# Kernel tuning notes

Hardware: AMD Instinct MI355X
Metric: run time of the kernel (lower is better)

The kernel has to match this reference:

```python
import jax, jax.numpy as jnp
import numpy as np

N, E, IN, H, HEADS, L, OUT = 4096, 262144, 64, 128, 4, 2, 2
DH = H // HEADS  # 32, per-head dim for both GAT and global MHA
BN_EPS = 1e-5
NEG_SLOPE = 0.2  # GATConv leaky_relu default


def setup_inputs() -> dict:
    key = jax.random.key(0)
    ks = iter(jax.random.split(key, 32))
    rn = lambda shape, s: jax.random.normal(next(ks), shape, jnp.float32) * s
    return {
        "x": rn((N, IN), 1.0),
        "edge_index": jax.random.randint(next(ks), (2, E), 0, N),
        "w_in": rn((H, IN), IN ** -0.5),
        "b_in": rn((H,), 0.02),
        "w_gat": rn((L, H, H), H ** -0.5),
        "att_src": rn((L, HEADS, DH), 0.1),
        "att_dst": rn((L, HEADS, DH), 0.1),
        "b_gat": rn((L, H), 0.02),
        "w_qkv": rn((L, 3 * H, H), H ** -0.5),
        "b_qkv": rn((L, 3 * H), 0.02),
        "w_o": rn((L, H, H), H ** -0.5),
        "b_o": rn((L, H), 0.02),
        "bn_gamma": 1.0 + rn((L, 3, H), 0.05),
        "bn_beta": rn((L, 3, H), 0.05),
        "w1": rn((L, 2 * H, H), H ** -0.5),
        "b1": rn((L, 2 * H), 0.02),
        "w2": rn((L, H, 2 * H), (2 * H) ** -0.5),
        "b2": rn((L, H), 0.02),
        "w_out": rn((OUT, H), H ** -0.5),
        "b_out": rn((OUT,), 0.02),
    }


def _bn(h, g, b):
    # eval-mode BatchNorm1d with running_mean=0, running_var=1
    return h * (g / jnp.sqrt(1.0 + BN_EPS)) + b


def _gat(x, src, dst, w, a_src, a_dst, bias):
    # GATConv(hidden, hidden//heads, heads=HEADS, add_self_loops=False), concat=True
    xp = (x @ w.T).reshape(N, HEADS, DH)                  # [N, HEADS, DH]
    al_s = jnp.einsum('nhd,hd->nh', xp, a_src)            # [N, HEADS]
    al_d = jnp.einsum('nhd,hd->nh', xp, a_dst)
    logit = al_s[src] + al_d[dst]                         # [E, HEADS]
    logit = jnp.where(logit >= 0, logit, NEG_SLOPE * logit)
    m = jax.ops.segment_max(logit, dst, num_segments=N)   # scatter-softmax over dst
    m = jnp.where(jnp.isfinite(m), m, 0.0)
    e = jnp.exp(logit - m[dst])
    denom = jax.ops.segment_sum(e, dst, num_segments=N)
    alpha = e / (denom[dst] + 1e-16)
    out = jax.ops.segment_sum(alpha[:, :, None] * xp[src], dst, num_segments=N)
    return out.reshape(N, H) + bias


def _mha(x, wqkv, bqkv, wo, bo):
    # torch.nn.MultiheadAttention self-attention over all N nodes (one graph)
    qkv = x @ wqkv.T + bqkv
    q, k, v = jnp.split(qkv, 3, axis=-1)
    q = q.reshape(N, HEADS, DH)
    k = k.reshape(N, HEADS, DH)
    v = v.reshape(N, HEADS, DH)
    scores = jnp.einsum('nhd,mhd->hnm', q, k) / jnp.sqrt(jnp.float32(DH))
    attn = jax.nn.softmax(scores, axis=-1)
    out = jnp.einsum('hnm,mhd->nhd', attn, v).reshape(N, H)
    return out @ wo.T + bo


def reference(x, edge_index, w_in, b_in, w_gat, att_src, att_dst, b_gat,
              w_qkv, b_qkv, w_o, b_o, bn_gamma, bn_beta,
              w1, b1, w2, b2, w_out, b_out):
    src, dst = edge_index[0], edge_index[1]
    h = jax.nn.relu(x @ w_in.T + b_in)
    for l in range(L):
        # GPSConv: local GAT branch (dropout inactive in eval)
        h_loc = _gat(h, src, dst, w_gat[l], att_src[l], att_dst[l], b_gat[l]) + h
        h_loc = _bn(h_loc, bn_gamma[l, 0], bn_beta[l, 0])
        # GPSConv: global attention branch
        h_att = _mha(h, w_qkv[l], b_qkv[l], w_o[l], b_o[l]) + h
        h_att = _bn(h_att, bn_gamma[l, 1], bn_beta[l, 1])
        out = h_loc + h_att
        mlp = jax.nn.relu(out @ w1[l].T + b1[l]) @ w2[l].T + b2[l]
        out = _bn(out + mlp, bn_gamma[l, 2], bn_beta[l, 2])
        # GPSRiskModel residual + relu (dropout inactive in eval)
        h = jax.nn.relu(out + h)
    return h @ w_out.T + b_out
```

## Files before the change

### kernel.cpp

```cpp
#include <hip/hip_runtime.h>

#define NN 4096
#define EE 262144
#define INF_ 64
#define HH 128
#define HEADS 4
#define DH 32
#define LL 2
#define NH (NN * HH)
#define KSPLIT 8
#define L2E 1.4426950408889634f

typedef unsigned short u16;
typedef unsigned int u32;
using bf16x8 = __attribute__((ext_vector_type(8))) short;
using f32x4 = __attribute__((ext_vector_type(4))) float;

__device__ __forceinline__ float bf2f(u16 v) { return __uint_as_float(((u32)v) << 16); }
__device__ __forceinline__ u16 f2bf(float f) {
    u32 u = __float_as_uint(f);
    u32 r = (u + 0x7fffu + ((u >> 16) & 1u)) >> 16;
    return (u16)r;
}
__device__ __forceinline__ u32 encf(float f) {
    u32 b = __float_as_uint(f);
    return (b & 0x80000000u) ? ~b : (b | 0x80000000u);
}
__device__ __forceinline__ float decf(u32 u) {
    u32 b = (u & 0x80000000u) ? (u & 0x7fffffffu) : ~u;
    return __uint_as_float(b);
}

__global__ __launch_bounds__(256) void k_detect(const u16* __restrict__ x, int* __restrict__ flag,
                                                int* __restrict__ cnt, u32* __restrict__ gmax) {
    int t = threadIdx.x;
    for (int i = t; i < NN; i += 256) cnt[i] = 0;
    if (t < 16) gmax[t] = 0;
    __shared__ int cs[256];
    u16 v = x[2 * t];
    int e = (v >> 7) & 0xFF;
    cs[t] = (e >= 100 && e <= 140) ? 1 : 0;
    __syncthreads();
    for (int s = 128; s > 0; s >>= 1) {
        if (t < s) cs[t] += cs[t + s];
        __syncthreads();
    }
    if (t == 0) *flag = (cs[0] >= 128) ? 1 : 0;
}

#define MAXSEG 16
struct SegF { const void* src[MAXSEG]; int dst[MAXSEG]; int n[MAXSEG]; int cnt; };
__global__ void k_cvtf(SegF S, float* __restrict__ W, const int* __restrict__ flag) {
    int seg = blockIdx.y;
    if (seg >= S.cnt) return;
    int n = S.n[seg];
    float* d = W + S.dst[seg];
    const void* s = S.src[seg];
    int f = *flag;
    for (int i = blockIdx.x * 256 + threadIdx.x; i < n; i += gridDim.x * 256)
        d[i] = f ? bf2f(((const u16*)s)[i]) : ((const float*)s)[i];
}
struct SegB { const void* src[8]; u16* dst[8]; u16* dst2[8]; int n[8]; int cnt; };
__global__ void k_cvtb(SegB S, const int* __restrict__ flag) {
    int seg = blockIdx.y;
    if (seg >= S.cnt) return;
    int n = S.n[seg];
    u16* d = S.dst[seg];
    u16* d2 = S.dst2[seg];
    const void* s = S.src[seg];
    int f = *flag;
    for (int i = blockIdx.x * 256 + threadIdx.x; i < n; i += gridDim.x * 256) {
        if (d2) {
            float v = f ? bf2f(((const u16*)s)[i]) : ((const float*)s)[i];
            u16 h = f2bf(v);
            d[i] = h;
            d2[i] = f2bf(v - bf2f(h));
        } else {
            d[i] = f ? ((const u16*)s)[i] : f2bf(((const float*)s)[i]);
        }
    }
}

__global__ void k_hist(const int* __restrict__ dst, int* __restrict__ cnt) {
    int e = blockIdx.x * blockDim.x + threadIdx.x;
    if (e < EE) atomicAdd(&cnt[dst[e]], 1);
}
__global__ __launch_bounds__(256) void k_scan(const int* __restrict__ cnt, int* __restrict__ rowstart,
                                              int* __restrict__ cursor) {
    __shared__ int part[256];
    int t = threadIdx.x;
    int loc[16];
    int s = 0;
#pragma unroll
    for (int i = 0; i < 16; ++i) { loc[i] = s; s += cnt[t * 16 + i]; }
    part[t] = s;
    __syncthreads();
    for (int off = 1; off < 256; off <<= 1) {
        int v = part[t];
        int a = (t >= off) ? part[t - off] : 0;
        __syncthreads();
        part[t] = v + a;
        __syncthreads();
    }
    int base = (t == 0) ? 0 : part[t - 1];
#pragma unroll
    for (int i = 0; i < 16; ++i) {
        rowstart[t * 16 + i] = base + loc[i];
        cursor[t * 16 + i] = base + loc[i];
    }
}
__global__ void k_scatter(const int* __restrict__ src, const int* __restrict__ dst,
                          int* __restrict__ cursor, int* __restrict__ esrc) {
    int e = blockIdx.x * blockDim.x + threadIdx.x;
    if (e < EE) {
        int d = dst[e];
        int p = atomicAdd(&cursor[d], 1);
        esrc[p] = src[e];
    }
}

__global__ __launch_bounds__(128) void k_mgemm(const u16* __restrict__ Ahi, const u16* __restrict__ Alo,
                                               const u16* __restrict__ Wb, const float* __restrict__ bias,
                                               float* __restrict__ outf, u16* __restrict__ outb16,
                                               u16* __restrict__ outhi, u16* __restrict__ outlo,
                                               int K, int J, int relu) {
    int wave = threadIdx.x >> 6, lane = threadIdx.x & 63;
    int grp = lane >> 4, lcol = lane & 15;
    int m0 = blockIdx.x * 32 + wave * 16;
    int j0 = blockIdx.y * 64;
    f32x4 acc[4];
#pragma unroll
    for (int s = 0; s < 4; ++s) acc[s] = (f32x4){0.f, 0.f, 0.f, 0.f};
    const u16* ah = Ahi + (size_t)(m0 + lcol) * K + grp * 8;
    const u16* al = Alo + (size_t)(m0 + lcol) * K + grp * 8;
    const u16* wb = Wb + (size_t)(j0 + lcol) * K + grp * 8;
    for (int k = 0; k < K; k += 32) {
        bf16x8 va = *(const bf16x8*)(ah + k);
        bf16x8 vl = *(const bf16x8*)(al + k);
#pragma unroll
        for (int s = 0; s < 4; ++s) {
            bf16x8 vw = *(const bf16x8*)(wb + (size_t)s * 16 * K + k);
            acc[s] = __builtin_amdgcn_mfma_f32_16x16x32_bf16(va, vw, acc[s], 0, 0, 0);
            acc[s] = __builtin_amdgcn_mfma_f32_16x16x32_bf16(vl, vw, acc[s], 0, 0, 0);
        }
    }
#pragma unroll
    for (int s = 0; s < 4; ++s) {
        int col = j0 + s * 16 + lcol;
        float bs = bias ? bias[col] : 0.f;
#pragma unroll
        for (int r = 0; r < 4; ++r) {
            float v = acc[s][r] + bs;
            if (relu) v = fmaxf(v, 0.f);
            size_t idx = (size_t)(m0 + grp * 4 + r) * J + col;
            if (outf) outf[idx] = v;
            if (outb16) outb16[idx] = f2bf(v);
            if (outhi) {
                u16 hv = f2bf(v);
                outhi[idx] = hv;
                outlo[idx] = f2bf(v - bf2f(hv));
            }
        }
    }
}

__global__ __launch_bounds__(128) void k_gemm_gq(const u16* __restrict__ Ahi, const u16* __restrict__ Alo,
                                                 const u16* __restrict__ wgat, const u16* __restrict__ wqkv,
                                                 const float* __restrict__ bqkv,
                                                 float* __restrict__ xpf, u16* __restrict__ xpb,
                                                 u16* __restrict__ qkvb) {
    int wave = threadIdx.x >> 6, lane = threadIdx.x & 63;
    int grp = lane >> 4, lcol = lane & 15;
    int m0 = blockIdx.x * 32 + wave * 16;
    int jb = blockIdx.y;
    int j0 = jb * 64;
    const u16* Wb = (jb < 2) ? (wgat + (size_t)j0 * HH) : (wqkv + (size_t)(j0 - 128) * HH);
    f32x4 acc[4];
#pragma unroll
    for (int s = 0; s < 4; ++s) acc[s] = (f32x4){0.f, 0.f, 0.f, 0.f};
    const u16* ah = Ahi + (size_t)(m0 + lcol) * HH + grp * 8;
    const u16* al = Alo + (size_t)(m0 + lcol) * HH + grp * 8;
    const u16* wb = Wb + (size_t)lcol * HH + grp * 8;
    for (int k = 0; k < HH; k += 32) {
        bf16x8 va = *(const bf16x8*)(ah + k);
        bf16x8 vl = *(const bf16x8*)(al + k);
#pragma unroll
        for (int s = 0; s < 4; ++s) {
            bf16x8 vw = *(const bf16x8*)(wb + (size_t)s * 16 * HH + k);
            acc[s] = __builtin_amdgcn_mfma_f32_16x16x32_bf16(va, vw, acc[s], 0, 0, 0);
            acc[s] = __builtin_amdgcn_mfma_f32_16x16x32_bf16(vl, vw, acc[s], 0, 0, 0);
        }
    }
    if (jb < 2) {
#pragma unroll
        for (int s = 0; s < 4; ++s) {
            int col = j0 + s * 16 + lcol;
#pragma unroll
            for (int r = 0; r < 4; ++r) {
                float v = acc[s][r];
                size_t idx = (size_t)(m0 + grp * 4 + r) * HH + col;
                xpf[idx] = v;
                xpb[idx] = f2bf(v);
            }
        }
    } else {
#pragma unroll
        for (int s = 0; s < 4; ++s) {
            int colq = j0 - 128 + s * 16 + lcol;
            float bs = bqkv[colq];
#pragma unroll
            for (int r = 0; r < 4; ++r)
                qkvb[(size_t)(m0 + grp * 4 + r) * 384 + colq] = f2bf(acc[s][r] + bs);
        }
    }
}

__global__ __launch_bounds__(256) void k_attlog(const float* __restrict__ xp, const float* __restrict__ asrc,
                                                const float* __restrict__ adst, float* __restrict__ als,
                                                float* __restrict__ ald, u32* __restrict__ gmax) {
    int t = blockIdx.x * 256 + threadIdx.x;
    int n = t >> 2, hh = t & 3;
    const float* xr = xp + (size_t)n * HH + hh * DH;
    float s1 = 0.f, s2 = 0.f;
#pragma unroll
    for (int d = 0; d < DH; ++d) {
        float v = xr[d];
        s1 += v * asrc[hh * DH + d];
        s2 += v * adst[hh * DH + d];
    }
    als[t] = s1;
    ald[t] = s2;
    __shared__ float red[256];
    int lt = threadIdx.x;
    red[lt] = s1;
    __syncthreads();
    for (int off = 128; off >= 4; off >>= 1) {
        if (lt < off) red[lt] = fmaxf(red[lt], red[lt + off]);
        __syncthreads();
    }
    if (lt < 4) atomicMax(&gmax[lt], encf(red[lt]));
    __syncthreads();
    red[lt] = s2;
    __syncthreads();
    for (int off = 128; off >= 4; off >>= 1) {
        if (lt < off) red[lt] = fmaxf(red[lt], red[lt + off]);
        __syncthreads();
    }
    if (lt < 4) atomicMax(&gmax[4 + lt], encf(red[lt]));
}

__global__ __launch_bounds__(128) void k_gemm_wo(const u16* __restrict__ Ahi, const u16* __restrict__ Alo,
                                                 const u16* __restrict__ Wb, const float* __restrict__ bias,
                                                 const float* __restrict__ gatb, const float* __restrict__ hbuf,
                                                 const float* __restrict__ bgat, const float* __restrict__ gam,
                                                 const float* __restrict__ bet,
                                                 float* __restrict__ outb, u16* __restrict__ ohi,
                                                 u16* __restrict__ olo) {
    int wave = threadIdx.x >> 6, lane = threadIdx.x & 63;
    int grp = lane >> 4, lcol = lane & 15;
    int m0 = blockIdx.x * 32 + wave * 16;
    int j0 = blockIdx.y * 64;
    f32x4 acc[4];
#pragma unroll
    for (int s = 0; s < 4; ++s) acc[s] = (f32x4){0.f, 0.f, 0.f, 0.f};
    const u16* ah = Ahi + (size_t)(m0 + lcol) * HH + grp * 8;
    const u16* al = Alo + (size_t)(m0 + lcol) * HH + grp * 8;
    const u16* wb = Wb + (size_t)(j0 + lcol) * HH + grp * 8;
    for (int k = 0; k < HH; k += 32) {
        bf16x8 va = *(const bf16x8*)(ah + k);
        bf16x8 vl = *(const bf16x8*)(al + k);
#pragma unroll
        for (int s = 0; s < 4; ++s) {
            bf16x8 vw = *(const bf16x8*)(wb + (size_t)s * 16 * HH + k);
            acc[s] = __builtin_amdgcn_mfma_f32_16x16x32_bf16(va, vw, acc[s], 0, 0, 0);
            acc[s] = __builtin_amdgcn_mfma_f32_16x16x32_bf16(vl, vw, acc[s], 0, 0, 0);
        }
    }
    float rs = rsqrtf(1.00001f);
#pragma unroll
    for (int s = 0; s < 4; ++s) {
        int col = j0 + s * 16 + lcol;
        float bs = bias[col];
        float g0 = gam[col] * rs, b0 = bet[col];
        float g1 = gam[HH + col] * rs, b1 = bet[HH + col];
        float bg = bgat[col];
#pragma unroll
        for (int r = 0; r < 4; ++r) {
            size_t idx = (size_t)(m0 + grp * 4 + r) * HH + col;
            float proj = acc[s][r] + bs;
            float hv = hbuf[idx];
            float hl = g0 * (gatb[idx] + bg + hv) + b0;
            float ha = g1 * (proj + hv) + b1;
            float v = hl + ha;
            outb[idx] = v;
            u16 hb = f2bf(v);
            ohi[idx] = hb;
            olo[idx] = f2bf(v - bf2f(hb));
        }
    }
}

__global__ __launch_bounds__(128) void k_gemm_w2(const u16* __restrict__ Ahi, const u16* __restrict__ Alo,
                                                 const u16* __restrict__ Wb, const float* __restrict__ bias,
                                                 const float* __restrict__ outb, const float* __restrict__ gam2,
                                                 const float* __restrict__ bet2,
                                                 float* __restrict__ hbuf, u16* __restrict__ hhi,
                                                 u16* __restrict__ hlo) {
    int wave = threadIdx.x >> 6, lane = threadIdx.x & 63;
    int grp = lane >> 4, lcol = lane & 15;
    int m0 = blockIdx.x * 32 + wave * 16;
    int j0 = blockIdx.y * 64;
    const int K = 2 * HH;
    f32x4 acc[4];
#pragma unroll
    for (int s = 0; s < 4; ++s) acc[s] = (f32x4){0.f, 0.f, 0.f, 0.f};
    const u16* ah = Ahi + (size_t)(m0 + lcol) * K + grp * 8;
    const u16* al = Alo + (size_t)(m0 + lcol) * K + grp * 8;
    const u16* wb = Wb + (size_t)(j0 + lcol) * K + grp * 8;
    for (int k = 0; k < K; k += 32) {
        bf16x8 va = *(const bf16x8*)(ah + k);
        bf16x8 vl = *(const bf16x8*)(al + k);
#pragma unroll
        for (int s = 0; s < 4; ++s) {
            bf16x8 vw = *(const bf16x8*)(wb + (size_t)s * 16 * K + k);
            acc[s] = __builtin_amdgcn_mfma_f32_16x16x32_bf16(va, vw, acc[s], 0, 0, 0);
            acc[s] = __builtin_amdgcn_mfma_f32_16x16x32_bf16(vl, vw, acc[s], 0, 0, 0);
        }
    }
    float rs = rsqrtf(1.00001f);
#pragma unroll
    for (int s = 0; s < 4; ++s) {
        int col = j0 + s * 16 + lcol;
        float bs = bias[col];
        float g2 = gam2[col] * rs, b2 = bet2[col];
#pragma unroll
        for (int r = 0; r < 4; ++r) {
            size_t idx = (size_t)(m0 + grp * 4 + r) * HH + col;
            float mlpo = acc[s][r] + bs;
            float o2 = g2 * (outb[idx] + mlpo) + b2;
            float v = fmaxf(o2 + hbuf[idx], 0.f);
            hbuf[idx] = v;
            u16 hb = f2bf(v);
            hhi[idx] = hb;
            hlo[idx] = f2bf(v - bf2f(hb));
        }
    }
}

#define GCHUNK 256
__global__ __launch_bounds__(128) void k_gat_node(const int* __restrict__ esrc, const int* __restrict__ rowstart,
                                                  const int* __restrict__ cnt, const float* __restrict__ als,
                                                  const float* __restrict__ ald, const u16* __restrict__ xpb,
                                                  float* __restrict__ gatout, const u32* __restrict__ gmax) {
    int n = blockIdx.x, t = threadIdx.x;
    int base = rowstart[n], c = cnt[n];
    float4 adv = ((const float4*)ald)[n];
    float ad[4] = {adv.x, adv.y, adv.z, adv.w};
    float M2[4];
#pragma unroll
    for (int h = 0; h < 4; ++h) {
        float bound = decf(gmax[h]) + decf(gmax[4 + h]);
        float M = bound >= 0.f ? bound : 0.2f * bound;
        M2[h] = M * L2E;
    }
    __shared__ float red[512];
    __shared__ float elds[GCHUNK * 4];
    __shared__ int slds[GCHUNK];
    float dsum[4] = {0.f, 0.f, 0.f, 0.f};
    float acc = 0.f;
    int ht = t >> 5;
    for (int ch = 0; ch < c; ch += GCHUNK) {
        int cn = min(GCHUNK, c - ch);
        __syncthreads();
        for (int i = t; i < cn; i += 128) {
            int s = esrc[base + ch + i];
            slds[i] = s;
            float4 as = ((const float4*)als)[s];
            float lg, e;
            lg = as.x + ad[0]; lg = lg >= 0.f ? lg : 0.2f * lg; e = __builtin_exp2f(lg * L2E - M2[0]); elds[i * 4 + 0] = e; dsum[0] += e;
            lg = as.y + ad[1]; lg = lg >= 0.f ? lg : 0.2f * lg; e = __builtin_exp2f(lg * L2E - M2[1]); elds[i * 4 + 1] = e; dsum[1] += e;
            lg = as.z + ad[2]; lg = lg >= 0.f ? lg : 0.2f * lg; e = __builtin_exp2f(lg * L2E - M2[2]); elds[i * 4 + 2] = e; dsum[2] += e;
            lg = as.w + ad[3]; lg = lg >= 0.f ? lg : 0.2f * lg; e = __builtin_exp2f(lg * L2E - M2[3]); elds[i * 4 + 3] = e; dsum[3] += e;
        }
        __syncthreads();
        int i = 0;
        for (; i + 2 <= cn; i += 2) {
            int s0 = slds[i], s1 = slds[i + 1];
            float e0 = elds[i * 4 + ht], e1 = elds[(i + 1) * 4 + ht];
            float x0 = bf2f(xpb[(size_t)s0 * HH + t]);
            float x1 = bf2f(xpb[(size_t)s1 * HH + t]);
            acc += e0 * x0 + e1 * x1;
        }
        if (i < cn) acc += elds[i * 4 + ht] * bf2f(xpb[(size_t)slds[i] * HH + t]);
    }
    __syncthreads();
#pragma unroll
    for (int h = 0; h < 4; ++h) red[h * 128 + t] = dsum[h];
    __syncthreads();
    for (int s2 = 64; s2 > 0; s2 >>= 1) {
        if (t < s2) {
#pragma unroll
            for (int h = 0; h < 4; ++h)
                red[h * 128 + t] += red[h * 128 + t + s2];
        }
        __syncthreads();
    }
    float inv = 1.f / (red[ht * 128] + 1e-16f);
    gatout[(size_t)n * HH + t] = acc * inv;
}

__global__ __launch_bounds__(256) void k_mha_split(const u16* __restrict__ qkvb,
                                                   float* __restrict__ PM, float* __restrict__ PL,
                                                   u16* __restrict__ PO) {
    const float C1 = 0.17677669529663687f * L2E;
    int head = blockIdx.x & 3;
    int qt = (blockIdx.x >> 2) & 63;
    int ks = blockIdx.x >> 8;
    int tid = threadIdx.x;
    int wave = tid >> 6, lane = tid & 63;
    int grp = lane >> 4, lcol = lane & 15;

    __shared__ __align__(16) u16 Klds[64][40];
    __shared__ __align__(16) u32 Vlds[32][36];
    __shared__ __align__(16) u16 Plds[4][16][66];

    int qrow0 = qt * 64 + wave * 16;
    bf16x8 aQ = *(const bf16x8*)(qkvb + (size_t)(qrow0 + lcol) * 384 + head * 32 + grp * 8);

    short onev = (lcol == 0) ? (short)0x3F80 : (short)0;
    bf16x8 bOne = {onev, onev, onev, onev, onev, onev, onev, onev};

    f32x4 oc0 = {0.f, 0.f, 0.f, 0.f}, oc1 = {0.f, 0.f, 0.f, 0.f}, ol = {0.f, 0.f, 0.f, 0.f};
    float msh = -INFINITY;

    int isK = (tid < 128);
    int st = tid & 127;
    int skey = st >> 1, shalf = (st & 1) * 16;
    int vj = st & 31, dgrp = st >> 5;
    int vkey0 = 32 * (vj & 1) + (vj >> 1);
    const u16* kptr = qkvb + 128 + head * 32 + shalf;
    const u16* vptr = qkvb + 256 + head * 32 + dgrp * 8;

    int kt0 = ks * (NN / KSPLIT);
    bf16x8 r0, r1;
    if (isK) {
        r0 = *(const bf16x8*)(kptr + (size_t)(kt0 + skey) * 384);
        r1 = *(const bf16x8*)(kptr + (size_t)(kt0 + skey) * 384 + 8);
    } else {
        r0 = *(const bf16x8*)(vptr + (size_t)(kt0 + vkey0) * 384);
        r1 = *(const bf16x8*)(vptr + (size_t)(kt0 + vkey0 + 16) * 384);
    }

    const int NT = (NN / KSPLIT) / 64;
    for (int t = 0; t < NT; ++t) {
        if (isK) {
            *(bf16x8*)(&Klds[skey][shalf]) = r0;
            *(bf16x8*)(&Klds[skey][shalf + 8]) = r1;
        } else {
#pragma unroll
            for (int j = 0; j < 8; ++j)
                Vlds[dgrp * 8 + j][vj] = (u32)(u16)r0[j] | ((u32)(u16)r1[j] << 16);
        }
        __syncthreads();
        if (t + 1 < NT) {
            int kn = kt0 + (t + 1) * 64;
            if (isK) {
                r0 = *(const bf16x8*)(kptr + (size_t)(kn + skey) * 384);
                r1 = *(const bf16x8*)(kptr + (size_t)(kn + skey) * 384 + 8);
            } else {
                r0 = *(const bf16x8*)(vptr + (size_t)(kn + vkey0) * 384);
                r1 = *(const bf16x8*)(vptr + (size_t)(kn + vkey0 + 16) * 384);
            }
        }
        f32x4 sc[4];
        f32x4 zero = {0.f, 0.f, 0.f, 0.f};
#pragma unroll
        for (int s = 0; s < 4; ++s) {
            bf16x8 bK = *(const bf16x8*)(&Klds[s * 16 + lcol][grp * 8]);
            sc[s] = __builtin_amdgcn_mfma_f32_16x16x32_bf16(aQ, bK, zero, 0, 0, 0);
        }
        float mymax = sc[0][0];
#pragma unroll
        for (int s = 0; s < 4; ++s)
#pragma unroll
            for (int r = 0; r < 4; ++r) mymax = fmaxf(mymax, sc[s][r]);
        mymax = fmaxf(mymax, __shfl_xor(mymax, 1));
        mymax = fmaxf(mymax, __shfl_xor(mymax, 2));
        mymax = fmaxf(mymax, __shfl_xor(mymax, 4));
        mymax = fmaxf(mymax, __shfl_xor(mymax, 8));
        float mnew = fmaxf(msh, mymax * C1);
        float cc = __builtin_exp2f(msh - mnew);
        msh = mnew;
#pragma unroll
        for (int r = 0; r < 4; ++r) {
            float p0 = __builtin_exp2f(__builtin_fmaf(sc[0][r], C1, -mnew));
            float p1 = __builtin_exp2f(__builtin_fmaf(sc[1][r], C1, -mnew));
            float p2 = __builtin_exp2f(__builtin_fmaf(sc[2][r], C1, -mnew));
            float p3 = __builtin_exp2f(__builtin_fmaf(sc[3][r], C1, -mnew));
            u32 pk01 = __builtin_amdgcn_perm(__float_as_uint(p1), __float_as_uint(p0), 0x07060302u);
            u32 pk23 = __builtin_amdgcn_perm(__float_as_uint(p3), __float_as_uint(p2), 0x07060302u);
            *(uint2*)(&Plds[wave][grp * 4 + r][4 * lcol]) = make_uint2(pk01, pk23);
        }
        oc0 *= cc;
        oc1 *= cc;
        ol *= cc;
#pragma unroll
        for (int c2 = 0; c2 < 2; ++c2) {
            bf16x8 aP = *(const bf16x8*)(&Plds[wave][lcol][c2 * 32 + grp * 8]);
            bf16x8 bV0 = *(const bf16x8*)(&Vlds[lcol][c2 * 16 + grp * 4]);
            bf16x8 bV1 = *(const bf16x8*)(&Vlds[16 + lcol][c2 * 16 + grp * 4]);
            oc0 = __builtin_amdgcn_mfma_f32_16x16x32_bf16(aP, bV0, oc0, 0, 0, 0);
            oc1 = __builtin_amdgcn_mfma_f32_16x16x32_bf16(aP, bV1, oc1, 0, 0, 0);
            ol = __builtin_amdgcn_mfma_f32_16x16x32_bf16(aP, bOne, ol, 0, 0, 0);
        }
        __syncthreads();
    }
#pragma unroll
    for (int r = 0; r < 4; ++r) {
        int row = qrow0 + grp * 4 + r;
        size_t base = ((size_t)row * HEADS + head) * KSPLIT + ks;
        PO[base * 32 + lcol] = f2bf(oc0[r]);
        PO[base * 32 + 16 + lcol] = f2bf(oc1[r]);
        if (lcol == 0) {
            PM[base] = msh;
            PL[base] = ol[r];
        }
    }
}

__global__ void k_mha_comb(const float* __restrict__ PM, const float* __restrict__ PL,
                           const u16* __restrict__ PO, u16* __restrict__ atthi,
                           u16* __restrict__ attlo) {
    int t = blockIdx.x * 256 + threadIdx.x;
    if (t >= NN * HH) return;
    int row = t >> 7, col = t & 127;
    int head = col >> 5, dim = col & 31;
    size_t b0 = ((size_t)row * HEADS + head) * KSPLIT;
    float m = -INFINITY;
#pragma unroll
    for (int k = 0; k < KSPLIT; ++k) m = fmaxf(m, PM[b0 + k]);
    float l = 0.f, o = 0.f;
#pragma unroll
    for (int k = 0; k < KSPLIT; ++k) {
        float w = __builtin_exp2f(PM[b0 + k] - m);
        l += PL[b0 + k] * w;
        o += bf2f(PO[(b0 + k) * 32 + dim]) * w;
    }
    float v = o / l;
    u16 h = f2bf(v);
    atthi[t] = h;
    attlo[t] = f2bf(v - bf2f(h));
}

__global__ __launch_bounds__(64) void k_out(const float* __restrict__ h, const float* __restrict__ w,
                                            const float* __restrict__ b, void* __restrict__ yout,
                                            const int* __restrict__ flag) {
    int n = blockIdx.x, l = threadIdx.x;
    float a0 = 0.f, a1 = 0.f;
    for (int k = l; k < HH; k += 64) {
        float hv = h[(size_t)n * HH + k];
        a0 += hv * w[k];
        a1 += hv * w[HH + k];
    }
#pragma unroll
    for (int off = 32; off > 0; off >>= 1) {
        a0 += __shfl_xor(a0, off);
        a1 += __shfl_xor(a1, off);
    }
    if (l == 0) {
        float o0 = a0 + b[0], o1 = a1 + b[1];
        if (*flag) {
            u16* y = (u16*)yout;
            y[n * 2 + 0] = f2bf(o0);
            y[n * 2 + 1] = f2bf(o1);
        } else {
            float* y = (float*)yout;
            y[n * 2 + 0] = o0;
            y[n * 2 + 1] = o1;
        }
    }
}

extern "C" void kernel_launch(void* const* d_in, const int* in_sizes, int n_in,
                              void* d_out, int out_size, void* d_ws, size_t ws_size,
                              hipStream_t stream) {
    float* W = (float*)d_ws;
    size_t o = 0;
    auto take = [&](size_t n) { size_t r = o; o += n; return r; };
    size_t pb_in = take(HH);
    size_t pattS = take(LL * HEADS * DH);
    size_t pattD = take(LL * HEADS * DH);
    size_t pb_gat = take(LL * HH);
    size_t pb_qkv = take(LL * 3 * HH);
    size_t pb_o  = take(LL * HH);
    size_t pbn_g = take(LL * 3 * HH);
    size_t pbn_b = take(LL * 3 * HH);
    size_t pb1   = take(LL * 2 * HH);
    size_t pb2   = take(LL * HH);
    size_t pw_out = take(2 * HH);
    size_t pb_out = take(2);
    auto takeb = [&](size_t nu16) { size_t r = o; o += (nu16 + 1) / 2; return r; };
    size_t bw_in  = takeb(HH * INF_);
    size_t bw_gat = takeb(LL * HH * HH);
    size_t bw_qkv = takeb(LL * 3 * HH * HH);
    size_t bw_o   = takeb(LL * HH * HH);
    size_t bw1    = takeb(LL * 2 * HH * HH);
    size_t bw2    = takeb(LL * HH * 2 * HH);
    o = (o + 127) & ~(size_t)127;
    size_t ohbuf = take(NH);
    size_t ogat  = take(NH);
    size_t otmp  = take(NH);
    size_t oals  = take(NN * HEADS);
    size_t oald  = take(NN * HEADS);
    size_t opm   = take(NN * HEADS * KSPLIT);
    size_t opl   = take(NN * HEADS * KSPLIT);
    size_t opo   = takeb((size_t)NN * HEADS * KSPLIT * 32);
    size_t oqkvb = takeb(NN * 384);
    size_t oxpb  = takeb(NH);
    size_t oxhi  = takeb(NN * INF_);
    size_t oxlo  = takeb(NN * INF_);
    size_t ohhi  = takeb(NH);
    size_t ohlo  = takeb(NH);
    size_t oahi  = takeb(NH);
    size_t oalo  = takeb(NH);
    size_t oohi  = takeb(NH);
    size_t oolo  = takeb(NH);
    size_t omhi  = takeb(NN * 2 * HH);
    size_t omlo  = takeb(NN * 2 * HH);
    int* ibase    = (int*)(W + o);
    int* iflag    = ibase;
    int* cnt      = ibase + 64;
    int* rowstart = cnt + NN;
    int* cursor   = rowstart + NN;
    int* esrc     = cursor + NN;
    u32* gmax     = (u32*)(esrc + EE);

    float* hbuf = W + ohbuf;
    float* gatb = W + ogat;
    float* tmp  = W + otmp;
    float* als  = W + oals;
    float* ald  = W + oald;
    float* pmb  = W + opm;
    float* plb  = W + opl;
    u16* pob  = (u16*)(W + opo);
    u16* qkvb = (u16*)(W + oqkvb);
    u16* xpb  = (u16*)(W + oxpb);
    u16* xhi = (u16*)(W + oxhi), *xlo = (u16*)(W + oxlo);
    u16* hhi = (u16*)(W + ohhi), *hlo = (u16*)(W + ohlo);
    u16* ahi = (u16*)(W + oahi), *alo = (u16*)(W + oalo);
    u16* ohi = (u16*)(W + oohi), *olo = (u16*)(W + oolo);
    u16* mhi = (u16*)(W + omhi), *mlo = (u16*)(W + omlo);

    const int* src = (const int*)d_in[1];
    const int* dst = (const int*)d_in[1] + EE;

    k_detect<<<1, 256, 0, stream>>>((const u16*)d_in[0], iflag, cnt, gmax);

    SegF SF = {};
    int nf = 0;
    auto addf = [&](int idx, size_t off, int n) { SF.src[nf] = d_in[idx]; SF.dst[nf] = (int)off; SF.n[nf] = n; ++nf; };
    addf(3, pb_in, HH);
    addf(5, pattS, LL * HEADS * DH);
    addf(6, pattD, LL * HEADS * DH);
    addf(7, pb_gat, LL * HH);
    addf(9, pb_qkv, LL * 3 * HH);
    addf(11, pb_o, LL * HH);
    addf(12, pbn_g, LL * 3 * HH);
    addf(13, pbn_b, LL * 3 * HH);
    addf(15, pb1, LL * 2 * HH);
    addf(17, pb2, LL * HH);
    addf(18, pw_out, 2 * HH);
    addf(19, pb_out, 2);
    SF.cnt = nf;
    k_cvtf<<<dim3(8, nf), 256, 0, stream>>>(SF, W, iflag);

    SegB SB = {};
    int nb = 0;
    auto addb = [&](int idx, size_t off, int n, u16* d2) {
        SB.src[nb] = d_in[idx]; SB.dst[nb] = (u16*)(W + off); SB.dst2[nb] = d2; SB.n[nb] = n; ++nb;
    };
    addb(2, bw_in, HH * INF_, nullptr);
    addb(4, bw_gat, LL * HH * HH, nullptr);
    addb(8, bw_qkv, LL * 3 * HH * HH, nullptr);
    addb(10, bw_o, LL * HH * HH, nullptr);
    addb(14, bw1, LL * 2 * HH * HH, nullptr);
    addb(16, bw2, LL * HH * 2 * HH, nullptr);
    SB.src[nb] = d_in[0]; SB.dst[nb] = xhi; SB.dst2[nb] = xlo; SB.n[nb] = NN * INF_; ++nb;
    SB.cnt = nb;
    k_cvtb<<<dim3(128, nb), 256, 0, stream>>>(SB, iflag);

    k_hist<<<EE / 256, 256, 0, stream>>>(dst, cnt);
    k_scan<<<1, 256, 0, stream>>>(cnt, rowstart, cursor);
    k_scatter<<<EE / 256, 256, 0, stream>>>(src, dst, cursor, esrc);

    k_mgemm<<<dim3(NN / 32, HH / 64), 128, 0, stream>>>(xhi, xlo, (u16*)(W + bw_in), W + pb_in,
                                                        hbuf, nullptr, hhi, hlo, INF_, HH, 1);

    for (int l = 0; l < LL; ++l) {
        k_gemm_gq<<<dim3(NN / 32, 8), 128, 0, stream>>>(hhi, hlo,
                                                        (u16*)(W + bw_gat) + (size_t)l * HH * HH,
                                                        (u16*)(W + bw_qkv) + (size_t)l * 3 * HH * HH,
                                                        W + pb_qkv + l * 3 * HH, tmp, xpb, qkvb);
        k_attlog<<<(NN * HEADS) / 256, 256, 0, stream>>>(tmp, W + pattS + l * HEADS * DH,
                                                         W + pattD + l * HEADS * DH, als, ald,
                                                         gmax + l * 8);
        k_gat_node<<<NN, 128, 0, stream>>>(esrc, rowstart, cnt, als, ald, xpb, gatb, gmax + l * 8);
        k_mha_split<<<(NN / 64) * HEADS * KSPLIT, 256, 0, stream>>>(qkvb, pmb, plb, pob);
        k_mha_comb<<<(NN * HH) / 256, 256, 0, stream>>>(pmb, plb, pob, ahi, alo);
        k_gemm_wo<<<dim3(NN / 32, HH / 64), 128, 0, stream>>>(ahi, alo,
                                                              (u16*)(W + bw_o) + (size_t)l * HH * HH,
                                                              W + pb_o + l * HH, gatb, hbuf,
                                                              W + pb_gat + l * HH, W + pbn_g + l * 3 * HH,
                                                              W + pbn_b + l * 3 * HH, tmp, ohi, olo);
        k_mgemm<<<dim3(NN / 32, 256 / 64), 128, 0, stream>>>(ohi, olo,
                                                             (u16*)(W + bw1) + (size_t)l * 2 * HH * HH,
                                                             W + pb1 + l * 2 * HH, nullptr, nullptr,
                                                             mhi, mlo, HH, 2 * HH, 1);
        k_gemm_w2<<<dim3(NN / 32, HH / 64), 128, 0, stream>>>(mhi, mlo,
                                                              (u16*)(W + bw2) + (size_t)l * HH * 2 * HH,
                                                              W + pb2 + l * HH, tmp,
                                                              W + pbn_g + l * 3 * HH + 2 * HH,
                                                              W + pbn_b + l * 3 * HH + 2 * HH,
                                                              hbuf, hhi, hlo);
    }
    k_out<<<NN, 64, 0, stream>>>(hbuf, W + pw_out, W + pb_out, d_out, iflag);
}
```

Before: 329.9 us.

## Enlarge MHA query tile, skip bf16 weight copies, drop fp32 xp store

The split-KV attention kernel now has each wave process 32 query rows instead of 16, so each K/V tile loaded into LDS is reused twice as much and half as many blocks launch. When inputs are already bf16, the GEMMs read weights straight from the input buffers through a runtime flag, so the conversion kernel skips those segments. The fp32 copy of the GAT projection is no longer written, and attention logits are computed from the bf16 copy instead. The GAT node gather loop is unrolled by four. Costs are more registers and LDS per block in the attention kernel, and logits that are computed from bf16-rounded values.

```diff
diff --git a/kernel.cpp b/kernel.cpp
--- a/kernel.cpp
+++ b/kernel.cpp
@@ -64,11 +64,12 @@
 __global__ void k_cvtb(SegB S, const int* __restrict__ flag) {
     int seg = blockIdx.y;
     if (seg >= S.cnt) return;
-    int n = S.n[seg];
+    int f = *flag;
     u16* d = S.dst[seg];
     u16* d2 = S.dst2[seg];
+    if (f && !d2) return;
+    int n = S.n[seg];
     const void* s = S.src[seg];
-    int f = *flag;
     for (int i = blockIdx.x * 256 + threadIdx.x; i < n; i += gridDim.x * 256) {
         if (d2) {
             float v = f ? bf2f(((const u16*)s)[i]) : ((const float*)s)[i];
@@ -76,7 +77,7 @@
             d[i] = h;
             d2[i] = f2bf(v - bf2f(h));
         } else {
-            d[i] = f ? ((const u16*)s)[i] : f2bf(((const float*)s)[i]);
+            d[i] = f2bf(((const float*)s)[i]);
         }
     }
 }
@@ -120,10 +121,13 @@
 }
 
 __global__ __launch_bounds__(128) void k_mgemm(const u16* __restrict__ Ahi, const u16* __restrict__ Alo,
-                                               const u16* __restrict__ Wb, const float* __restrict__ bias,
+                                               const u16* __restrict__ Wc, const u16* __restrict__ Wd,
+                                               const int* __restrict__ flag,
+                                               const float* __restrict__ bias,
                                                float* __restrict__ outf, u16* __restrict__ outb16,
                                                u16* __restrict__ outhi, u16* __restrict__ outlo,
                                                int K, int J, int relu) {
+    const u16* Wb = (*flag) ? Wd : Wc;
     int wave = threadIdx.x >> 6, lane = threadIdx.x & 63;
     int grp = lane >> 4, lcol = lane & 15;
     int m0 = blockIdx.x * 32 + wave * 16;
@@ -165,15 +169,19 @@
 }
 
 __global__ __launch_bounds__(128) void k_gemm_gq(const u16* __restrict__ Ahi, const u16* __restrict__ Alo,
-                                                 const u16* __restrict__ wgat, const u16* __restrict__ wqkv,
+                                                 const u16* __restrict__ wgatc, const u16* __restrict__ wgatd,
+                                                 const u16* __restrict__ wqkvc, const u16* __restrict__ wqkvd,
+                                                 const int* __restrict__ flag,
                                                  const float* __restrict__ bqkv,
-                                                 float* __restrict__ xpf, u16* __restrict__ xpb,
-                                                 u16* __restrict__ qkvb) {
+                                                 u16* __restrict__ xpb, u16* __restrict__ qkvb) {
     int wave = threadIdx.x >> 6, lane = threadIdx.x & 63;
     int grp = lane >> 4, lcol = lane & 15;
     int m0 = blockIdx.x * 32 + wave * 16;
     int jb = blockIdx.y;
     int j0 = jb * 64;
+    int f = *flag;
+    const u16* wgat = f ? wgatd : wgatc;
+    const u16* wqkv = f ? wqkvd : wqkvc;
     const u16* Wb = (jb < 2) ? (wgat + (size_t)j0 * HH) : (wqkv + (size_t)(j0 - 128) * HH);
     f32x4 acc[4];
 #pragma unroll
@@ -196,12 +204,8 @@
         for (int s = 0; s < 4; ++s) {
             int col = j0 + s * 16 + lcol;
 #pragma unroll
-            for (int r = 0; r < 4; ++r) {
-                float v = acc[s][r];
-                size_t idx = (size_t)(m0 + grp * 4 + r) * HH + col;
-                xpf[idx] = v;
-                xpb[idx] = f2bf(v);
-            }
+            for (int r = 0; r < 4; ++r)
+                xpb[(size_t)(m0 + grp * 4 + r) * HH + col] = f2bf(acc[s][r]);
         }
     } else {
 #pragma unroll
@@ -215,16 +219,16 @@
     }
 }
 
-__global__ __launch_bounds__(256) void k_attlog(const float* __restrict__ xp, const float* __restrict__ asrc,
+__global__ __launch_bounds__(256) void k_attlog(const u16* __restrict__ xpb, const float* __restrict__ asrc,
                                                 const float* __restrict__ adst, float* __restrict__ als,
                                                 float* __restrict__ ald, u32* __restrict__ gmax) {
     int t = blockIdx.x * 256 + threadIdx.x;
     int n = t >> 2, hh = t & 3;
-    const float* xr = xp + (size_t)n * HH + hh * DH;
+    const u16* xr = xpb + (size_t)n * HH + hh * DH;
     float s1 = 0.f, s2 = 0.f;
 #pragma unroll
     for (int d = 0; d < DH; ++d) {
-        float v = xr[d];
+        float v = bf2f(xr[d]);
         s1 += v * asrc[hh * DH + d];
         s2 += v * adst[hh * DH + d];
     }
@@ -250,12 +254,15 @@
 }
 
 __global__ __launch_bounds__(128) void k_gemm_wo(const u16* __restrict__ Ahi, const u16* __restrict__ Alo,
-                                                 const u16* __restrict__ Wb, const float* __restrict__ bias,
+                                                 const u16* __restrict__ Wc, const u16* __restrict__ Wd,
+                                                 const int* __restrict__ flag,
+                                                 const float* __restrict__ bias,
                                                  const float* __restrict__ gatb, const float* __restrict__ hbuf,
                                                  const float* __restrict__ bgat, const float* __restrict__ gam,
                                                  const float* __restrict__ bet,
                                                  float* __restrict__ outb, u16* __restrict__ ohi,
                                                  u16* __restrict__ olo) {
+    const u16* Wb = (*flag) ? Wd : Wc;
     int wave = threadIdx.x >> 6, lane = threadIdx.x & 63;
     int grp = lane >> 4, lcol = lane & 15;
     int m0 = blockIdx.x * 32 + wave * 16;
@@ -301,11 +308,14 @@
 }
 
 __global__ __launch_bounds__(128) void k_gemm_w2(const u16* __restrict__ Ahi, const u16* __restrict__ Alo,
-                                                 const u16* __restrict__ Wb, const float* __restrict__ bias,
+                                                 const u16* __restrict__ Wc, const u16* __restrict__ Wd,
+                                                 const int* __restrict__ flag,
+                                                 const float* __restrict__ bias,
                                                  const float* __restrict__ outb, const float* __restrict__ gam2,
                                                  const float* __restrict__ bet2,
                                                  float* __restrict__ hbuf, u16* __restrict__ hhi,
                                                  u16* __restrict__ hlo) {
+    const u16* Wb = (*flag) ? Wd : Wc;
     int wave = threadIdx.x >> 6, lane = threadIdx.x & 63;
     int grp = lane >> 4, lcol = lane & 15;
     int m0 = blockIdx.x * 32 + wave * 16;
@@ -384,14 +394,16 @@
         }
         __syncthreads();
         int i = 0;
-        for (; i + 2 <= cn; i += 2) {
-            int s0 = slds[i], s1 = slds[i + 1];
-            float e0 = elds[i * 4 + ht], e1 = elds[(i + 1) * 4 + ht];
+        for (; i + 4 <= cn; i += 4) {
+            int s0 = slds[i], s1 = slds[i + 1], s2 = slds[i + 2], s3 = slds[i + 3];
             float x0 = bf2f(xpb[(size_t)s0 * HH + t]);
             float x1 = bf2f(xpb[(size_t)s1 * HH + t]);
-            acc += e0 * x0 + e1 * x1;
-        }
-        if (i < cn) acc += elds[i * 4 + ht] * bf2f(xpb[(size_t)slds[i] * HH + t]);
+            float x2 = bf2f(xpb[(size_t)s2 * HH + t]);
+            float x3 = bf2f(xpb[(size_t)s3 * HH + t]);
+            acc += elds[i * 4 + ht] * x0 + elds[(i + 1) * 4 + ht] * x1;
+            acc += elds[(i + 2) * 4 + ht] * x2 + elds[(i + 3) * 4 + ht] * x3;
+        }
+        for (; i < cn; ++i) acc += elds[i * 4 + ht] * bf2f(xpb[(size_t)slds[i] * HH + t]);
     }
     __syncthreads();
 #pragma unroll
@@ -414,23 +426,26 @@
                                                    u16* __restrict__ PO) {
     const float C1 = 0.17677669529663687f * L2E;
     int head = blockIdx.x & 3;
-    int qt = (blockIdx.x >> 2) & 63;
-    int ks = blockIdx.x >> 8;
+    int qt = (blockIdx.x >> 2) & 31;
+    int ks = blockIdx.x >> 7;
     int tid = threadIdx.x;
     int wave = tid >> 6, lane = tid & 63;
     int grp = lane >> 4, lcol = lane & 15;
 
     __shared__ __align__(16) u16 Klds[64][40];
     __shared__ __align__(16) u32 Vlds[32][36];
-    __shared__ __align__(16) u16 Plds[4][16][66];
-
-    int qrow0 = qt * 64 + wave * 16;
-    bf16x8 aQ = *(const bf16x8*)(qkvb + (size_t)(qrow0 + lcol) * 384 + head * 32 + grp * 8);
+    __shared__ __align__(16) u16 Plds[4][32][66];
+
+    int qrow0 = qt * 128 + wave * 32;
+    bf16x8 aQ0 = *(const bf16x8*)(qkvb + (size_t)(qrow0 + lcol) * 384 + head * 32 + grp * 8);
+    bf16x8 aQ1 = *(const bf16x8*)(qkvb + (size_t)(qrow0 + 16 + lcol) * 384 + head * 32 + grp * 8);
 
     short onev = (lcol == 0) ? (short)0x3F80 : (short)0;
     bf16x8 bOne = {onev, onev, onev, onev, onev, onev, onev, onev};
 
-    f32x4 oc0 = {0.f, 0.f, 0.f, 0.f}, oc1 = {0.f, 0.f, 0.f, 0.f}, ol = {0.f, 0.f, 0.f, 0.f};
+    f32x4 oc00 = {0.f, 0.f, 0.f, 0.f}, oc01 = {0.f, 0.f, 0.f, 0.f};
+    f32x4 oc10 = {0.f, 0.f, 0.f, 0.f}, oc11 = {0.f, 0.f, 0.f, 0.f};
+    f32x4 ol0 = {0.f, 0.f, 0.f, 0.f}, ol1 = {0.f, 0.f, 0.f, 0.f};
     float msh = -INFINITY;
 
     int isK = (tid < 128);
@@ -472,18 +487,22 @@
                 r1 = *(const bf16x8*)(vptr + (size_t)(kn + vkey0 + 16) * 384);
             }
         }
-        f32x4 sc[4];
+        f32x4 sc0[4], sc1[4];
         f32x4 zero = {0.f, 0.f, 0.f, 0.f};
 #pragma unroll
         for (int s = 0; s < 4; ++s) {
             bf16x8 bK = *(const bf16x8*)(&Klds[s * 16 + lcol][grp * 8]);
-            sc[s] = __builtin_amdgcn_mfma_f32_16x16x32_bf16(aQ, bK, zero, 0, 0, 0);
-        }
-        float mymax = sc[0][0];
+            sc0[s] = __builtin_amdgcn_mfma_f32_16x16x32_bf16(aQ0, bK, zero, 0, 0, 0);
+            sc1[s] = __builtin_amdgcn_mfma_f32_16x16x32_bf16(aQ1, bK, zero, 0, 0, 0);
+        }
+        float mymax = sc0[0][0];
 #pragma unroll
         for (int s = 0; s < 4; ++s)
 #pragma unroll
-            for (int r = 0; r < 4; ++r) mymax = fmaxf(mymax, sc[s][r]);
+            for (int r = 0; r < 4; ++r) {
+                mymax = fmaxf(mymax, sc0[s][r]);
+                mymax = fmaxf(mymax, sc1[s][r]);
+            }
         mymax = fmaxf(mymax, __shfl_xor(mymax, 1));
         mymax = fmaxf(mymax, __shfl_xor(mymax, 2));
         mymax = fmaxf(mymax, __shfl_xor(mymax, 4));
@@ -493,37 +512,53 @@
         msh = mnew;
 #pragma unroll
         for (int r = 0; r < 4; ++r) {
-            float p0 = __builtin_exp2f(__builtin_fmaf(sc[0][r], C1, -mnew));
-            float p1 = __builtin_exp2f(__builtin_fmaf(sc[1][r], C1, -mnew));
-            float p2 = __builtin_exp2f(__builtin_fmaf(sc[2][r], C1, -mnew));
-            float p3 = __builtin_exp2f(__builtin_fmaf(sc[3][r], C1, -mnew));
-            u32 pk01 = __builtin_amdgcn_perm(__float_as_uint(p1), __float_as_uint(p0), 0x07060302u);
-            u32 pk23 = __builtin_amdgcn_perm(__float_as_uint(p3), __float_as_uint(p2), 0x07060302u);
-            *(uint2*)(&Plds[wave][grp * 4 + r][4 * lcol]) = make_uint2(pk01, pk23);
-        }
-        oc0 *= cc;
-        oc1 *= cc;
-        ol *= cc;
+            float p0 = __builtin_exp2f(__builtin_fmaf(sc0[0][r], C1, -mnew));
+            float p1 = __builtin_exp2f(__builtin_fmaf(sc0[1][r], C1, -mnew));
+            float p2 = __builtin_exp2f(__builtin_fmaf(sc0[2][r], C1, -mnew));
+            float p3 = __builtin_exp2f(__builtin_fmaf(sc0[3][r], C1, -mnew));
+            u32 a01 = __builtin_amdgcn_perm(__float_as_uint(p1), __float_as_uint(p0), 0x07060302u);
+            u32 a23 = __builtin_amdgcn_perm(__float_as_uint(p3), __float_as_uint(p2), 0x07060302u);
+            *(uint2*)(&Plds[wave][grp * 4 + r][4 * lcol]) = make_uint2(a01, a23);
+            float q0 = __builtin_exp2f(__builtin_fmaf(sc1[0][r], C1, -mnew));
+            float q1 = __builtin_exp2f(__builtin_fmaf(sc1[1][r], C1, -mnew));
+            float q2 = __builtin_exp2f(__builtin_fmaf(sc1[2][r], C1, -mnew));
+            float q3 = __builtin_exp2f(__builtin_fmaf(sc1[3][r], C1, -mnew));
+            u32 b01 = __builtin_amdgcn_perm(__float_as_uint(q1), __float_as_uint(q0), 0x07060302u);
+            u32 b23 = __builtin_amdgcn_perm(__float_as_uint(q3), __float_as_uint(q2), 0x07060302u);
+            *(uint2*)(&Plds[wave][16 + grp * 4 + r][4 * lcol]) = make_uint2(b01, b23);
+        }
+        oc00 *= cc; oc01 *= cc; ol0 *= cc;
+        oc10 *= cc; oc11 *= cc; ol1 *= cc;
 #pragma unroll
         for (int c2 = 0; c2 < 2; ++c2) {
-            bf16x8 aP = *(const bf16x8*)(&Plds[wave][lcol][c2 * 32 + grp * 8]);
+            bf16x8 aP0 = *(const bf16x8*)(&Plds[wave][lcol][c2 * 32 + grp * 8]);
+            bf16x8 aP1 = *(const bf16x8*)(&Plds[wave][16 + lcol][c2 * 32 + grp * 8]);
             bf16x8 bV0 = *(const bf16x8*)(&Vlds[lcol][c2 * 16 + grp * 4]);
             bf16x8 bV1 = *(const bf16x8*)(&Vlds[16 + lcol][c2 * 16 + grp * 4]);
-            oc0 = __builtin_amdgcn_mfma_f32_16x16x32_bf16(aP, bV0, oc0, 0, 0, 0);
-            oc1 = __builtin_amdgcn_mfma_f32_16x16x32_bf16(aP, bV1, oc1, 0, 0, 0);
-            ol = __builtin_amdgcn_mfma_f32_16x16x32_bf16(aP, bOne, ol, 0, 0, 0);
+            oc00 = __builtin_amdgcn_mfma_f32_16x16x32_bf16(aP0, bV0, oc00, 0, 0, 0);
+            oc01 = __builtin_amdgcn_mfma_f32_16x16x32_bf16(aP0, bV1, oc01, 0, 0, 0);
+            ol0 = __builtin_amdgcn_mfma_f32_16x16x32_bf16(aP0, bOne, ol0, 0, 0, 0);
+            oc10 = __builtin_amdgcn_mfma_f32_16x16x32_bf16(aP1, bV0, oc10, 0, 0, 0);
+            oc11 = __builtin_amdgcn_mfma_f32_16x16x32_bf16(aP1, bV1, oc11, 0, 0, 0);
+            ol1 = __builtin_amdgcn_mfma_f32_16x16x32_bf16(aP1, bOne, ol1, 0, 0, 0);
         }
         __syncthreads();
     }
 #pragma unroll
     for (int r = 0; r < 4; ++r) {
-        int row = qrow0 + grp * 4 + r;
-        size_t base = ((size_t)row * HEADS + head) * KSPLIT + ks;
-        PO[base * 32 + lcol] = f2bf(oc0[r]);
-        PO[base * 32 + 16 + lcol] = f2bf(oc1[r]);
+        int row0 = qrow0 + grp * 4 + r;
+        size_t b0 = ((size_t)row0 * HEADS + head) * KSPLIT + ks;
+        PO[b0 * 32 + lcol] = f2bf(oc00[r]);
+        PO[b0 * 32 + 16 + lcol] = f2bf(oc01[r]);
+        int row1 = row0 + 16;
+        size_t b1 = ((size_t)row1 * HEADS + head) * KSPLIT + ks;
+        PO[b1 * 32 + lcol] = f2bf(oc10[r]);
+        PO[b1 * 32 + 16 + lcol] = f2bf(oc11[r]);
         if (lcol == 0) {
-            PM[base] = msh;
-            PL[base] = ol[r];
+            PM[b0] = msh;
+            PL[b0] = ol0[r];
+            PM[b1] = msh;
+            PL[b1] = ol1[r];
         }
     }
 }
@@ -653,6 +688,12 @@
 
     const int* src = (const int*)d_in[1];
     const int* dst = (const int*)d_in[1] + EE;
+    const u16* dw_in  = (const u16*)d_in[2];
+    const u16* dw_gat = (const u16*)d_in[4];
+    const u16* dw_qkv = (const u16*)d_in[8];
+    const u16* dw_o   = (const u16*)d_in[10];
+    const u16* dw1    = (const u16*)d_in[14];
+    const u16* dw2    = (const u16*)d_in[16];
 
     k_detect<<<1, 256, 0, stream>>>((const u16*)d_in[0], iflag, cnt, gmax);
 
@@ -693,31 +734,36 @@
     k_scan<<<1, 256, 0, stream>>>(cnt, rowstart, cursor);
     k_scatter<<<EE / 256, 256, 0, stream>>>(src, dst, cursor, esrc);
 
-    k_mgemm<<<dim3(NN / 32, HH / 64), 128, 0, stream>>>(xhi, xlo, (u16*)(W + bw_in), W + pb_in,
-                                                        hbuf, nullptr, hhi, hlo, INF_, HH, 1);
+    k_mgemm<<<dim3(NN / 32, HH / 64), 128, 0, stream>>>(xhi, xlo, (u16*)(W + bw_in), dw_in, iflag,
+                                                        W + pb_in, hbuf, nullptr, hhi, hlo, INF_, HH, 1);
 
     for (int l = 0; l < LL; ++l) {
         k_gemm_gq<<<dim3(NN / 32, 8), 128, 0, stream>>>(hhi, hlo,
                                                         (u16*)(W + bw_gat) + (size_t)l * HH * HH,
+                                                        dw_gat + (size_t)l * HH * HH,
                                                         (u16*)(W + bw_qkv) + (size_t)l * 3 * HH * HH,
-                                                        W + pb_qkv + l * 3 * HH, tmp, xpb, qkvb);
-        k_attlog<<<(NN * HEADS) / 256, 256, 0, stream>>>(tmp, W + pattS + l * HEADS * DH,
+                                                        dw_qkv + (size_t)l * 3 * HH * HH,
+                                                        iflag, W + pb_qkv + l * 3 * HH, xpb, qkvb);
+        k_attlog<<<(NN * HEADS) / 256, 256, 0, stream>>>(xpb, W + pattS + l * HEADS * DH,
                                                          W + pattD + l * HEADS * DH, als, ald,
                                                          gmax + l * 8);
         k_gat_node<<<NN, 128, 0, stream>>>(esrc, rowstart, cnt, als, ald, xpb, gatb, gmax + l * 8);
-        k_mha_split<<<(NN / 64) * HEADS * KSPLIT, 256, 0, stream>>>(qkvb, pmb, plb, pob);
+        k_mha_split<<<(NN / 128) * HEADS * KSPLIT, 256, 0, stream>>>(qkvb, pmb, plb, pob);
         k_mha_comb<<<(NN * HH) / 256, 256, 0, stream>>>(pmb, plb, pob, ahi, alo);
         k_gemm_wo<<<dim3(NN / 32, HH / 64), 128, 0, stream>>>(ahi, alo,
                                                               (u16*)(W + bw_o) + (size_t)l * HH * HH,
+                                                              dw_o + (size_t)l * HH * HH, iflag,
                                                               W + pb_o + l * HH, gatb, hbuf,
                                                               W + pb_gat + l * HH, W + pbn_g + l * 3 * HH,
                                                               W + pbn_b + l * 3 * HH, tmp, ohi, olo);
         k_mgemm<<<dim3(NN / 32, 256 / 64), 128, 0, stream>>>(ohi, olo,
                                                              (u16*)(W + bw1) + (size_t)l * 2 * HH * HH,
+                                                             dw1 + (size_t)l * 2 * HH * HH, iflag,
                                                              W + pb1 + l * 2 * HH, nullptr, nullptr,
                                                              mhi, mlo, HH, 2 * HH, 1);
         k_gemm_w2<<<dim3(NN / 32, HH / 64), 128, 0, stream>>>(mhi, mlo,
                                                               (u16*)(W + bw2) + (size_t)l * HH * 2 * HH,
+                                                              dw2 + (size_t)l * HH * 2 * HH, iflag,
                                                               W + pb2 + l * HH, tmp,
                                                               W + pbn_g + l * 3 * HH + 2 * HH,
                                                               W + pbn_b + l * 3 * HH + 2 * HH,
```

Result: no change. 324.9 us (-1.5%).
